# Kernel optimization log

Hardware: AMD Instinct MI355X
Metric: run time of the kernel (lower is better)

Reference implementation:

```python
import jax, jax.numpy as jnp
import numpy as np

EPS = 1e-5

def _ada_ln(x, c, W_ss, b_ss):
    # LayerNorm without affine, then conditional scale/bias from c via SiLU->Linear
    mu = jnp.mean(x, axis=-1, keepdims=True)
    var = jnp.mean((x - mu) ** 2, axis=-1, keepdims=True)
    h = (x - mu) / jnp.sqrt(var + EPS)
    ss = jax.nn.silu(c) @ W_ss + b_ss            # [B, 2H]
    scale, bias = jnp.split(ss, 2, axis=-1)      # [B, H] each
    return (1.0 + scale)[:, None, :] * h + bias[:, None, :]

def setup_inputs() -> dict:
    key = jax.random.key(0)
    ks = jax.random.split(key, 12)
    B, Lq, Lkv, H = 8, 2048, 512, 1024
    s = 0.02
    return {
        "x_q": jax.random.normal(ks[0], (B, Lq, H), jnp.float32),
        "x_kv": jax.random.normal(ks[1], (B, Lkv, H), jnp.float32),
        "t_vec": jax.random.normal(ks[2], (B, H), jnp.float32),
        "Wq": jax.random.normal(ks[3], (H, H), jnp.float32) * s,
        "bq": jnp.zeros((H,), jnp.float32),
        "Wkv": jax.random.normal(ks[4], (H, 2 * H), jnp.float32) * s,
        "bkv": jnp.zeros((2 * H,), jnp.float32),
        "Wp": jax.random.normal(ks[5], (H, H), jnp.float32) * s,
        "bp": jnp.zeros((H,), jnp.float32),
        "Wss_q": jax.random.normal(ks[6], (H, 2 * H), jnp.float32) * s,
        "bss_q": jnp.zeros((2 * H,), jnp.float32),
        "Wss_kv": jax.random.normal(ks[7], (H, 2 * H), jnp.float32) * s,
        "bss_kv": jnp.zeros((2 * H,), jnp.float32),
    }

def reference(x_q, x_kv, t_vec, Wq, bq, Wkv, bkv, Wp, bp, Wss_q, bss_q, Wss_kv, bss_kv):
    B, Lq, H = x_q.shape
    Lkv = x_kv.shape[1]
    nh = 16
    dh = H // nh

    xq = _ada_ln(x_q, t_vec, Wss_q, bss_q)
    xkv = _ada_ln(x_kv, t_vec, Wss_kv, bss_kv)

    q = (xq @ Wq + bq).reshape(B, Lq, nh, dh)          # [B,Lq,h,d]
    kv = (xkv @ Wkv + bkv).reshape(B, Lkv, 2, nh, dh)
    k = kv[:, :, 0]                                     # [B,Lkv,h,d]
    v = kv[:, :, 1]

    scores = jnp.einsum("bqhd,bkhd->bhqk", q, k) / jnp.sqrt(jnp.float32(dh))
    attn = jax.nn.softmax(scores, axis=-1)
    out = jnp.einsum("bhqk,bkhd->bqhd", attn, v).reshape(B, Lq, H)
    return x_q + (out @ Wp + bp)
```

## Files before the change

### kernel.cpp

```cpp
#include <hip/hip_runtime.h>
#include <hip/hip_bf16.h>
#include <stdint.h>

typedef __attribute__((ext_vector_type(8))) short bf16x8;
typedef __attribute__((ext_vector_type(4))) float f32x4;
typedef __attribute__((ext_vector_type(4))) _Float16 f16x4;
typedef __attribute__((ext_vector_type(8))) _Float16 f16x8;
typedef __attribute__((ext_vector_type(4))) unsigned short u16x4;

__device__ __forceinline__ float b2f(unsigned short u){
  union { unsigned int i; float f; } x; x.i = ((unsigned int)u) << 16; return x.f;
}
__device__ __forceinline__ unsigned short f2b(float f){
  union { float f; unsigned int i; } x; x.f = f;
  unsigned int r = x.i + 0x7fffu + ((x.i >> 16) & 1u);
  return (unsigned short)(r >> 16);
}

__device__ __forceinline__ void gld_lds16(const void* g, void* l){
  __builtin_amdgcn_global_load_lds((const __attribute__((address_space(1))) unsigned int*)g,
                                   (__attribute__((address_space(3))) unsigned int*)l,
                                   16, 0, 0);
}

__global__ __launch_bounds__(256) void transpose_k(const float* __restrict__ in,
                                                   unsigned short* __restrict__ out,
                                                   int R, int C){
  __shared__ unsigned short tile[32][33];
  int tx = threadIdx.x & 31, ty = threadIdx.x >> 5;
  int r0 = blockIdx.y * 32, c0 = blockIdx.x * 32;
#pragma unroll
  for (int t = 0; t < 4; ++t)
    tile[ty + t*8][tx] = f2b(in[(size_t)(r0 + ty + t*8) * C + c0 + tx]);
  __syncthreads();
#pragma unroll
  for (int t = 0; t < 4; ++t)
    out[(size_t)(c0 + ty + t*8) * R + r0 + tx] = tile[tx][ty + t*8];
}

__global__ __launch_bounds__(256) void ss_init_k(const float* __restrict__ bssq,
                                                 const float* __restrict__ bssk,
                                                 float* __restrict__ ss_q,
                                                 float* __restrict__ ss_kv){
  int idx = blockIdx.x*256 + threadIdx.x;
  int which = idx >> 14, rem = idx & 16383;
  int j = rem & 2047;
  if (which) ss_kv[rem] = bssk[j];
  else       ss_q[rem]  = bssq[j];
}

__global__ __launch_bounds__(256) void ss2_k(const float* __restrict__ tvec,
                                             const float* __restrict__ Wssq,
                                             const float* __restrict__ Wssk,
                                             float* __restrict__ ss_q,
                                             float* __restrict__ ss_kv){
  const int which = blockIdx.z;
  const float* W = which ? Wssk : Wssq;
  float* ss = which ? ss_kv : ss_q;
  const int col = blockIdx.x*256 + threadIdx.x;
  const int k0 = blockIdx.y*64;

  __shared__ float sl[8][64];
  int idx = threadIdx.x;
#pragma unroll
  for (int t = 0; t < 2; ++t){
    int i = idx + t*256;
    int b = i >> 6, k = i & 63;
    float c = tvec[b*1024 + k0 + k];
    sl[b][k] = c / (1.f + __expf(-c));
  }
  __syncthreads();

  float acc[8] = {0.f,0.f,0.f,0.f,0.f,0.f,0.f,0.f};
#pragma unroll 8
  for (int k = 0; k < 64; ++k){
    float w = W[(size_t)(k0 + k)*2048 + col];
#pragma unroll
    for (int b = 0; b < 8; ++b) acc[b] += sl[b][k] * w;
  }
#pragma unroll
  for (int b = 0; b < 8; ++b)
    atomicAdd(&ss[b*2048 + col], acc[b]);
}

__global__ __launch_bounds__(256) void ada_ln_k(const float* __restrict__ x,
                                                const float* __restrict__ ss,
                                                unsigned short* __restrict__ out,
                                                int L){
  int row = blockIdx.x;
  int b = row / L;
  const float* xr = x + (size_t)row * 1024;
  int tid = threadIdx.x;
  float4 v = *(const float4*)&xr[tid*4];
  float s = v.x + v.y + v.z + v.w;
  __shared__ float red[4];
#pragma unroll
  for (int o = 32; o > 0; o >>= 1) s += __shfl_xor(s, o, 64);
  if ((tid & 63) == 0) red[tid >> 6] = s;
  __syncthreads();
  float mu = (red[0]+red[1]+red[2]+red[3]) * (1.f/1024.f);
  __syncthreads();
  float vs = (v.x-mu)*(v.x-mu) + (v.y-mu)*(v.y-mu) + (v.z-mu)*(v.z-mu) + (v.w-mu)*(v.w-mu);
#pragma unroll
  for (int o = 32; o > 0; o >>= 1) vs += __shfl_xor(vs, o, 64);
  if ((tid & 63) == 0) red[tid >> 6] = vs;
  __syncthreads();
  float var = (red[0]+red[1]+red[2]+red[3]) * (1.f/1024.f);
  float inv = rsqrtf(var + 1e-5f);
  const float* sb = ss + (size_t)b*2048;
  float4 sc = *(const float4*)&sb[tid*4];
  float4 bi = *(const float4*)&sb[1024 + tid*4];
  u16x4 o4;
  o4[0] = f2b((1.f + sc.x) * ((v.x-mu)*inv) + bi.x);
  o4[1] = f2b((1.f + sc.y) * ((v.y-mu)*inv) + bi.y);
  o4[2] = f2b((1.f + sc.z) * ((v.z-mu)*inv) + bi.z);
  o4[3] = f2b((1.f + sc.w) * ((v.w-mu)*inv) + bi.w);
  *(u16x4*)&out[(size_t)row*1024 + tid*4] = o4;
}

__global__ __launch_bounds__(256) void gemm_bt_k(const unsigned short* __restrict__ A,
                                                 const unsigned short* __restrict__ BT,
                                                 const float* __restrict__ bias,
                                                 const float* __restrict__ resf,
                                                 unsigned short* __restrict__ Cb,
                                                 float* __restrict__ Cf,
                                                 _Float16* __restrict__ vT,
                                                 int M, int N, int K, int mode){
  __shared__ __attribute__((aligned(16))) unsigned short As[2][128*64];
  __shared__ __attribute__((aligned(16))) unsigned short Bs[2][128*64];
  const int tid = threadIdx.x;
  const int wave = tid >> 6, lane = tid & 63;
  const int lm = lane & 15, quad = lane >> 4;

  const int gx = gridDim.x;
  const int nwg = gx * gridDim.y;
  const int lid = blockIdx.y * gx + blockIdx.x;
  const int chunk = nwg >> 3;
  const int tile = (lid & 7) * chunk + (lid >> 3);
  const int m0 = (tile / gx) * 128, n0 = (tile % gx) * 128;

  const int wm = (wave >> 1) * 64, wn = (wave & 1) * 64;
  f32x4 acc[4][4];
#pragma unroll
  for (int i = 0; i < 4; ++i)
#pragma unroll
    for (int j = 0; j < 4; ++j) acc[i][j] = (f32x4){0.f,0.f,0.f,0.f};

  int rowc[4], colc[4];
#pragma unroll
  for (int r = 0; r < 4; ++r){
    int c = r*256 + tid;
    rowc[r] = c >> 3; colc[r] = (c & 7) * 8;
  }

#define STAGE128(buf, kk)                                                              \
  {                                                                                    \
    _Pragma("unroll")                                                                  \
    for (int r = 0; r < 4; ++r)                                                        \
      gld_lds16(&A[(size_t)(m0 + rowc[r])*K + (kk) + colc[r]], &As[buf][(r*256 + tid)*8]); \
    _Pragma("unroll")                                                                  \
    for (int r = 0; r < 4; ++r)                                                        \
      gld_lds16(&BT[(size_t)(n0 + rowc[r])*K + (kk) + colc[r]], &Bs[buf][(r*256 + tid)*8]); \
  }

  const int NT = K >> 6;
  STAGE128(0, 0);
  STAGE128(1, 64);
  asm volatile("s_waitcnt vmcnt(8)" ::: "memory");
  __builtin_amdgcn_s_barrier();

  for (int t = 0; t < NT; ++t){
    const int cur = t & 1;
#pragma unroll
    for (int ks = 0; ks < 2; ++ks){
      bf16x8 af[4], bfr[4];
#pragma unroll
      for (int i = 0; i < 4; ++i)
        af[i] = *(bf16x8*)&As[cur][(wm + i*16 + lm)*64 + ks*32 + quad*8];
#pragma unroll
      for (int j = 0; j < 4; ++j)
        bfr[j] = *(bf16x8*)&Bs[cur][(wn + j*16 + lm)*64 + ks*32 + quad*8];
#pragma unroll
      for (int i = 0; i < 4; ++i)
#pragma unroll
        for (int j = 0; j < 4; ++j)
          acc[i][j] = __builtin_amdgcn_mfma_f32_16x16x32_bf16(af[i], bfr[j], acc[i][j], 0, 0, 0);
    }
    if (t + 1 < NT){
      __builtin_amdgcn_s_barrier();
      if (t + 2 < NT){
        STAGE128(cur, (t + 2) << 6);
        asm volatile("s_waitcnt vmcnt(8)" ::: "memory");
      } else {
        asm volatile("s_waitcnt vmcnt(0)" ::: "memory");
      }
      __builtin_amdgcn_s_barrier();
    }
  }
#undef STAGE128

  if (mode == 2 && n0 >= 1024){
#pragma unroll
    for (int j = 0; j < 4; ++j){
      int col = n0 + wn + j*16 + lm;
      int d = col - 1024;
      float bv = bias[col];
#pragma unroll
      for (int i = 0; i < 4; ++i){
        int rowb = m0 + wm + i*16 + quad*4;
        int brow = rowb >> 9, l = rowb & 511;
        f16x4 h4;
#pragma unroll
        for (int p = 0; p < 4; ++p) h4[p] = (_Float16)(acc[i][j][p] + bv);
        *(f16x4*)&vT[((size_t)brow*1024 + d)*512 + l] = h4;
      }
    }
    return;
  }

#pragma unroll
  for (int j = 0; j < 4; ++j){
    int col = n0 + wn + j*16 + lm;
    float bv = bias[col];
#pragma unroll
    for (int i = 0; i < 4; ++i){
#pragma unroll
      for (int p = 0; p < 4; ++p){
        int row = m0 + wm + i*16 + quad*4 + p;
        float v = acc[i][j][p] + bv;
        if (mode == 1){
          Cf[(size_t)row*N + col] = v + resf[(size_t)row*N + col];
        } else {
          Cb[(size_t)row*1024 + col] = f2b(v);
        }
      }
    }
  }
}

__global__ __launch_bounds__(512) void gemm256_k(const unsigned short* __restrict__ A,
                                                 const unsigned short* __restrict__ BT,
                                                 const float* __restrict__ bias,
                                                 const float* __restrict__ resf,
                                                 unsigned short* __restrict__ Cb,
                                                 float* __restrict__ Cf,
                                                 int M, int N, int K, int mode){
  __shared__ __attribute__((aligned(16))) unsigned short As[2][2][8192];
  __shared__ __attribute__((aligned(16))) unsigned short Bs[2][2][8192];
  const int tid = threadIdx.x;
  const int wave = tid >> 6, lane = tid & 63;
  const int lm = lane & 15, quad = lane >> 4;

  const int gx = gridDim.x;
  const int nwg = gx * gridDim.y;
  const int lid = blockIdx.y * gx + blockIdx.x;
  const int chunkw = nwg >> 3;
  const int tileid = (lid & 7) * chunkw + (lid >> 3);
  const int m0 = (tileid / gx) * 256, n0 = (tileid % gx) * 256;

  const int wm = (wave >> 2) * 128, wn = (wave & 3) * 64;

  f32x4 acc[8][4];
#pragma unroll
  for (int i = 0; i < 8; ++i)
#pragma unroll
    for (int j = 0; j < 4; ++j) acc[i][j] = (f32x4){0.f,0.f,0.f,0.f};

  int srow[2], scol0[2];
#pragma unroll
  for (int r = 0; r < 2; ++r){
    int lc = r*512 + tid;
    srow[r]  = lc >> 2;
    scol0[r] = ((lc & 3) ^ ((srow[r] >> 1) & 3)) << 3;
  }

#define STG_A(bufb, ksb, kt)                                                            \
  { _Pragma("unroll")                                                                   \
    for (int r = 0; r < 2; ++r)                                                         \
      gld_lds16(&A[(size_t)(m0 + srow[r])*K + (kt)*64 + (ksb)*32 + scol0[r]],           \
                &As[bufb][ksb][(r*512 + tid)*8]); }
#define STG_B(bufb, ksb, kt)                                                            \
  { _Pragma("unroll")                                                                   \
    for (int r = 0; r < 2; ++r)                                                         \
      gld_lds16(&BT[(size_t)(n0 + srow[r])*K + (kt)*64 + (ksb)*32 + scol0[r]],          \
                &Bs[bufb][ksb][(r*512 + tid)*8]); }

  const int rc = (quad ^ ((lm >> 1) & 3)) * 8;
  const int arow = (wm + lm)*32 + rc;
  const int brow = (wn + lm)*32 + rc;

#define PHASE(bufb, mh, ksb, STAGES, VM)                                                \
  { bf16x8 af[4], bfr[4];                                                               \
    _Pragma("unroll")                                                                   \
    for (int i = 0; i < 4; ++i)                                                         \
      af[i] = *(const bf16x8*)&As[bufb][ksb][arow + ((mh)*4 + i)*512];                  \
    _Pragma("unroll")                                                                   \
    for (int j = 0; j < 4; ++j)                                                         \
      bfr[j] = *(const bf16x8*)&Bs[bufb][ksb][brow + j*512];                            \
    STAGES;                                                                             \
    __builtin_amdgcn_s_barrier();                                                       \
    __builtin_amdgcn_s_setprio(1);                                                      \
    _Pragma("unroll")                                                                   \
    for (int i = 0; i < 4; ++i)                                                         \
      _Pragma("unroll")                                                                 \
      for (int j = 0; j < 4; ++j)                                                       \
        acc[(mh)*4 + i][j] =                                                            \
          __builtin_amdgcn_mfma_f32_16x16x32_bf16(af[i], bfr[j], acc[(mh)*4 + i][j], 0, 0, 0); \
    __builtin_amdgcn_s_setprio(0);                                                      \
    VM;                                                                                 \
    __builtin_amdgcn_s_barrier(); }

  const int NT = K >> 6;
  const int NU = NT >> 1;

  STG_A(0, 0, 0); STG_B(0, 0, 0);
  STG_A(0, 1, 0); STG_B(0, 1, 0);
  STG_A(1, 0, 1); STG_B(1, 0, 1);
  asm volatile("s_waitcnt vmcnt(8)" ::: "memory");
  __builtin_amdgcn_s_barrier();

  for (int u = 0; u < NU; ++u){
    const int t1 = 2*u + 1, t2 = 2*u + 2, t3 = 2*u + 3;
    const bool nlast = (u + 1 < NU);
    PHASE(0, 0, 0, { STG_A(1, 1, t1); }, {});
    PHASE(0, 1, 0, { STG_B(1, 1, t1); },
          { asm volatile("s_waitcnt vmcnt(8)" ::: "memory"); });
    PHASE(0, 0, 1, { if (nlast) STG_A(0, 0, t2); }, {});
    PHASE(0, 1, 1, { if (nlast) STG_B(0, 0, t2); },
          { if (nlast) asm volatile("s_waitcnt vmcnt(8)" ::: "memory");
            else       asm volatile("s_waitcnt vmcnt(4)" ::: "memory"); });
    PHASE(1, 0, 0, { if (nlast) STG_A(0, 1, t2); }, {});
    PHASE(1, 1, 0, { if (nlast) STG_B(0, 1, t2); },
          { if (nlast) asm volatile("s_waitcnt vmcnt(8)" ::: "memory");
            else       asm volatile("s_waitcnt vmcnt(0)" ::: "memory"); });
    PHASE(1, 0, 1, { if (nlast) STG_A(1, 0, t3); }, {});
    PHASE(1, 1, 1, { if (nlast) STG_B(1, 0, t3); },
          { if (nlast) asm volatile("s_waitcnt vmcnt(8)" ::: "memory"); });
  }
#undef PHASE
#undef STG_A
#undef STG_B

#pragma unroll
  for (int j = 0; j < 4; ++j){
    int col = n0 + wn + j*16 + lm;
    float bv = bias[col];
#pragma unroll
    for (int i = 0; i < 8; ++i){
#pragma unroll
      for (int p = 0; p < 4; ++p){
        int row = m0 + wm + i*16 + quad*4 + p;
        float v = acc[i][j][p] + bv;
        if (mode == 1){
          Cf[(size_t)row*N + col] = v + resf[(size_t)row*N + col];
        } else {
          Cb[(size_t)row*1024 + col] = f2b(v);
        }
      }
    }
  }
}

__global__ __launch_bounds__(256) void attn_k(const unsigned short* __restrict__ q,
                                              const unsigned short* __restrict__ kbuf,
                                              const _Float16* __restrict__ vT,
                                              unsigned short* __restrict__ out){
  const int lid = (blockIdx.z * gridDim.y + blockIdx.y) * gridDim.x + blockIdx.x;
  const int tile = (lid & 7) * 256 + (lid >> 3);
  const int qb = tile & 15, h = (tile >> 4) & 15, b = tile >> 8;
  const int tid = threadIdx.x;
  const int wave = tid >> 6, lane = tid & 63;
  const int lm = lane & 15, quad = lane >> 4;
  const int q0 = qb * 128;

  __shared__ __attribute__((aligned(16))) unsigned short Ks[64*72];
  __shared__ __attribute__((aligned(16))) _Float16      Vs[64*72];

  bf16x8 qf[2][2];
#pragma unroll
  for (int u = 0; u < 2; ++u){
    const unsigned short* qrow = q + ((size_t)b*2048 + q0 + wave*32 + u*16 + lm)*1024 + h*64;
    qf[u][0] = *(const bf16x8*)&qrow[quad*8];
    qf[u][1] = *(const bf16x8*)&qrow[32 + quad*8];
  }

  const unsigned short* kb = kbuf + ((size_t)b*512)*1024 + h*64;
  const _Float16*       vb = vT + ((size_t)b*1024 + h*64)*512;

  f32x4 oacc[2][4];
#pragma unroll
  for (int u = 0; u < 2; ++u)
#pragma unroll
    for (int nt = 0; nt < 4; ++nt) oacc[u][nt] = (f32x4){0.f,0.f,0.f,0.f};
  float m_run[2] = {-1e30f, -1e30f}, l_run[2] = {0.f, 0.f};

  const int srow = tid >> 3, scol = (tid & 7) * 8;

  for (int kt = 0; kt < 8; ++kt){
    const int l0 = kt * 64;
    __syncthreads();
#pragma unroll
    for (int r = 0; r < 2; ++r){
      int row = r*32 + srow;
      *(bf16x8*)&Ks[row*72 + scol] = *(const bf16x8*)&kb[(size_t)(l0 + row)*1024 + scol];
      *(f16x8*)&Vs[row*72 + scol]  = *(const f16x8*)&vb[(size_t)row*512 + l0 + scol];
    }
    __syncthreads();

    f32x4 sacc[2][4];
#pragma unroll
    for (int u = 0; u < 2; ++u)
#pragma unroll
      for (int s = 0; s < 4; ++s) sacc[u][s] = (f32x4){0.f,0.f,0.f,0.f};
#pragma unroll
    for (int s = 0; s < 4; ++s){
      bf16x8 kf0 = *(bf16x8*)&Ks[(s*16 + lm)*72 + quad*8];
      bf16x8 kf1 = *(bf16x8*)&Ks[(s*16 + lm)*72 + 32 + quad*8];
#pragma unroll
      for (int u = 0; u < 2; ++u){
        sacc[u][s] = __builtin_amdgcn_mfma_f32_16x16x32_bf16(kf0, qf[u][0], sacc[u][s], 0, 0, 0);
        sacc[u][s] = __builtin_amdgcn_mfma_f32_16x16x32_bf16(kf1, qf[u][1], sacc[u][s], 0, 0, 0);
      }
    }

    f16x4 pf[2][4];
#pragma unroll
    for (int u = 0; u < 2; ++u){
      float tm = -1e30f;
#pragma unroll
      for (int s = 0; s < 4; ++s)
#pragma unroll
        for (int p = 0; p < 4; ++p) tm = fmaxf(tm, sacc[u][s][p]);
      tm = fmaxf(tm, __shfl_xor(tm, 16, 64));
      tm = fmaxf(tm, __shfl_xor(tm, 32, 64));
      float m_new = fmaxf(m_run[u], tm * 0.125f);
      float alpha = __expf(m_run[u] - m_new);
      m_run[u] = m_new;
      l_run[u] *= alpha;
      float ap[4];
#pragma unroll
      for (int p = 0; p < 4; ++p) ap[p] = __shfl(alpha, quad*4 + p, 64);
#pragma unroll
      for (int nt = 0; nt < 4; ++nt){
        oacc[u][nt][0] *= ap[0]; oacc[u][nt][1] *= ap[1];
        oacc[u][nt][2] *= ap[2]; oacc[u][nt][3] *= ap[3];
      }
#pragma unroll
      for (int s = 0; s < 4; ++s)
#pragma unroll
        for (int p = 0; p < 4; ++p){
          float e = __expf(sacc[u][s][p] * 0.125f - m_new);
          l_run[u] += e;
          pf[u][s][p] = (_Float16)e;
        }
    }

#pragma unroll
    for (int s = 0; s < 4; ++s){
#pragma unroll
      for (int nt = 0; nt < 4; ++nt){
        f16x4 vf = *(const f16x4*)&Vs[(size_t)(nt*16 + lm)*72 + s*16 + quad*4];
#pragma unroll
        for (int u = 0; u < 2; ++u)
          oacc[u][nt] = __builtin_amdgcn_mfma_f32_16x16x16f16(pf[u][s], vf, oacc[u][nt], 0, 0, 0);
      }
    }
  }

#pragma unroll
  for (int u = 0; u < 2; ++u){
    float lr = l_run[u];
    lr += __shfl_xor(lr, 16, 64);
    lr += __shfl_xor(lr, 32, 64);
    float rinv = 1.f / lr;
    float rp[4];
#pragma unroll
    for (int p = 0; p < 4; ++p) rp[p] = __shfl(rinv, quad*4 + p, 64);
    const size_t obase = ((size_t)b*2048 + q0 + wave*32 + u*16) * 1024 + h*64;
#pragma unroll
    for (int nt = 0; nt < 4; ++nt)
#pragma unroll
      for (int p = 0; p < 4; ++p){
        int row = quad*4 + p;
        out[obase + (size_t)row*1024 + nt*16 + lm] = f2b(oacc[u][nt][p] * rp[p]);
      }
  }
}

extern "C" void kernel_launch(void* const* d_in, const int* in_sizes, int n_in,
                              void* d_out, int out_size, void* d_ws, size_t ws_size,
                              hipStream_t stream){
  const float* x_q  = (const float*)d_in[0];
  const float* x_kv = (const float*)d_in[1];
  const float* tvec = (const float*)d_in[2];
  const float* Wq   = (const float*)d_in[3];
  const float* bq   = (const float*)d_in[4];
  const float* Wkv  = (const float*)d_in[5];
  const float* bkv  = (const float*)d_in[6];
  const float* Wp   = (const float*)d_in[7];
  const float* bp   = (const float*)d_in[8];
  const float* Wssq = (const float*)d_in[9];
  const float* bssq = (const float*)d_in[10];
  const float* Wssk = (const float*)d_in[11];
  const float* bssk = (const float*)d_in[12];

  char* ws = (char*)d_ws;
  float*          ss_q  = (float*)(ws + 0);
  float*          ss_kv = (float*)(ws + 65536);
  unsigned short* xq    = (unsigned short*)(ws + 131072);
  unsigned short* xkv   = (unsigned short*)(ws + 33685504);
  unsigned short* qbuf  = (unsigned short*)(ws + 42074112);
  unsigned short* kbuf  = (unsigned short*)(ws + 75628544);
  _Float16*       vTbuf = (_Float16*)     (ws + 84017152);
  unsigned short* WqT   = (unsigned short*)(ws + 92405760);
  unsigned short* WkvT  = (unsigned short*)(ws + 94502912);
  unsigned short* WpT   = (unsigned short*)(ws + 98697216);

  dim3 blk(256);
  transpose_k<<<dim3(32, 32), blk, 0, stream>>>(Wq,  WqT,  1024, 1024);
  transpose_k<<<dim3(64, 32), blk, 0, stream>>>(Wkv, WkvT, 1024, 2048);
  transpose_k<<<dim3(32, 32), blk, 0, stream>>>(Wp,  WpT,  1024, 1024);

  ss_init_k<<<dim3(128), blk, 0, stream>>>(bssq, bssk, ss_q, ss_kv);
  ss2_k<<<dim3(8, 16, 2), blk, 0, stream>>>(tvec, Wssq, Wssk, ss_q, ss_kv);

  ada_ln_k<<<dim3(16384), blk, 0, stream>>>(x_q,  ss_q,  xq,  2048);
  ada_ln_k<<<dim3(4096),  blk, 0, stream>>>(x_kv, ss_kv, xkv, 512);

  gemm256_k<<<dim3(4, 64), dim3(512), 0, stream>>>(xq, WqT, bq, nullptr, qbuf, nullptr,
                                                   16384, 1024, 1024, 0);
  gemm_bt_k<<<dim3(16, 32), blk, 0, stream>>>(xkv, WkvT, bkv, nullptr, kbuf, nullptr, vTbuf,
                                              4096, 2048, 1024, 2);

  attn_k<<<dim3(16, 16, 8), blk, 0, stream>>>(qbuf, kbuf, vTbuf, xq);

  gemm256_k<<<dim3(4, 64), dim3(512), 0, stream>>>(xq, WpT, bp, x_q, nullptr, (float*)d_out,
                                                   16384, 1024, 1024, 1);
}
```

Before: 415.2 us.

## Double-buffer K/V tiles via register prefetch and skip unneeded softmax rescale

The attention kernel now prefetches the next K/V tile from global memory into registers while the current tile is being processed. Shared memory is split into two buffers, and the row stride changes from 72 to 76 elements, which alters the bank-conflict pattern. The online-softmax rescale of the output accumulators is skipped whenever no lane's running max increases. Together these aim to hide global load latency and cut redundant exp and multiply work, at the cost of extra registers and LDS per block, which may reduce occupancy.

```diff
diff --git a/kernel.cpp b/kernel.cpp
--- a/kernel.cpp
+++ b/kernel.cpp
@@ -373,8 +373,8 @@
   const int lm = lane & 15, quad = lane >> 4;
   const int q0 = qb * 128;
 
-  __shared__ __attribute__((aligned(16))) unsigned short Ks[64*72];
-  __shared__ __attribute__((aligned(16))) _Float16      Vs[64*72];
+  __shared__ __attribute__((aligned(16))) unsigned short Ks[2][64*76];
+  __shared__ __attribute__((aligned(16))) _Float16      Vs[2][64*76];
 
   bf16x8 qf[2][2];
 #pragma unroll
@@ -396,14 +396,32 @@
 
   const int srow = tid >> 3, scol = (tid & 7) * 8;
 
+  bf16x8 kreg[2];
+  f16x8  vreg[2];
+#pragma unroll
+  for (int r = 0; r < 2; ++r){
+    int row = r*32 + srow;
+    kreg[r] = *(const bf16x8*)&kb[(size_t)row*1024 + scol];
+    vreg[r] = *(const f16x8*)&vb[(size_t)row*512 + scol];
+  }
+
   for (int kt = 0; kt < 8; ++kt){
-    const int l0 = kt * 64;
+    const int buf = kt & 1;
     __syncthreads();
 #pragma unroll
     for (int r = 0; r < 2; ++r){
       int row = r*32 + srow;
-      *(bf16x8*)&Ks[row*72 + scol] = *(const bf16x8*)&kb[(size_t)(l0 + row)*1024 + scol];
-      *(f16x8*)&Vs[row*72 + scol]  = *(const f16x8*)&vb[(size_t)row*512 + l0 + scol];
+      *(bf16x8*)&Ks[buf][row*76 + scol] = kreg[r];
+      *(f16x8*)&Vs[buf][row*76 + scol]  = vreg[r];
+    }
+    if (kt + 1 < 8){
+      const int l1 = (kt + 1) * 64;
+#pragma unroll
+      for (int r = 0; r < 2; ++r){
+        int row = r*32 + srow;
+        kreg[r] = *(const bf16x8*)&kb[(size_t)(l1 + row)*1024 + scol];
+        vreg[r] = *(const f16x8*)&vb[(size_t)row*512 + l1 + scol];
+      }
     }
     __syncthreads();
 
@@ -414,8 +432,8 @@
       for (int s = 0; s < 4; ++s) sacc[u][s] = (f32x4){0.f,0.f,0.f,0.f};
 #pragma unroll
     for (int s = 0; s < 4; ++s){
-      bf16x8 kf0 = *(bf16x8*)&Ks[(s*16 + lm)*72 + quad*8];
-      bf16x8 kf1 = *(bf16x8*)&Ks[(s*16 + lm)*72 + 32 + quad*8];
+      bf16x8 kf0 = *(bf16x8*)&Ks[buf][(s*16 + lm)*76 + quad*8];
+      bf16x8 kf1 = *(bf16x8*)&Ks[buf][(s*16 + lm)*76 + 32 + quad*8];
 #pragma unroll
       for (int u = 0; u < 2; ++u){
         sacc[u][s] = __builtin_amdgcn_mfma_f32_16x16x32_bf16(kf0, qf[u][0], sacc[u][s], 0, 0, 0);
@@ -433,23 +451,26 @@
         for (int p = 0; p < 4; ++p) tm = fmaxf(tm, sacc[u][s][p]);
       tm = fmaxf(tm, __shfl_xor(tm, 16, 64));
       tm = fmaxf(tm, __shfl_xor(tm, 32, 64));
-      float m_new = fmaxf(m_run[u], tm * 0.125f);
-      float alpha = __expf(m_run[u] - m_new);
-      m_run[u] = m_new;
-      l_run[u] *= alpha;
-      float ap[4];
-#pragma unroll
-      for (int p = 0; p < 4; ++p) ap[p] = __shfl(alpha, quad*4 + p, 64);
-#pragma unroll
-      for (int nt = 0; nt < 4; ++nt){
-        oacc[u][nt][0] *= ap[0]; oacc[u][nt][1] *= ap[1];
-        oacc[u][nt][2] *= ap[2]; oacc[u][nt][3] *= ap[3];
+      tm *= 0.125f;
+      if (__any(tm > m_run[u])){
+        float m_new = fmaxf(m_run[u], tm);
+        float alpha = __expf(m_run[u] - m_new);
+        m_run[u] = m_new;
+        l_run[u] *= alpha;
+        float ap[4];
+#pragma unroll
+        for (int p = 0; p < 4; ++p) ap[p] = __shfl(alpha, quad*4 + p, 64);
+#pragma unroll
+        for (int nt = 0; nt < 4; ++nt){
+          oacc[u][nt][0] *= ap[0]; oacc[u][nt][1] *= ap[1];
+          oacc[u][nt][2] *= ap[2]; oacc[u][nt][3] *= ap[3];
+        }
       }
 #pragma unroll
       for (int s = 0; s < 4; ++s)
 #pragma unroll
         for (int p = 0; p < 4; ++p){
-          float e = __expf(sacc[u][s][p] * 0.125f - m_new);
+          float e = __expf(sacc[u][s][p] * 0.125f - m_run[u]);
           l_run[u] += e;
           pf[u][s][p] = (_Float16)e;
         }
@@ -459,7 +480,7 @@
     for (int s = 0; s < 4; ++s){
 #pragma unroll
       for (int nt = 0; nt < 4; ++nt){
-        f16x4 vf = *(const f16x4*)&Vs[(size_t)(nt*16 + lm)*72 + s*16 + quad*4];
+        f16x4 vf = *(const f16x4*)&Vs[buf][(size_t)(nt*16 + lm)*76 + s*16 + quad*4];
 #pragma unroll
         for (int u = 0; u < 2; ++u)
           oacc[u][nt] = __builtin_amdgcn_mfma_f32_16x16x16f16(pf[u][s], vf, oacc[u][nt], 0, 0, 0);
```

Result: no change. 414.8 us (-0.1%).
